# Kernel optimization log

Measured on AMD Instinct MI355X. Metric: run time of the kernel, lower is better.

Reference implementation:

```python
import jax, jax.numpy as jnp
import numpy as np

B, T = 4, 15
NY = NX = 256
RES = 0.05
LAT0 = 32.0
G = 9.81
F0 = 1e-4
C0 = 2.7
DT = 21600.0
TINT = 86400.0
NSTEP = int(TINT // DT)  # 4 Euler sub-steps

# --- grid spacing: mean of dx, dy as in lonlat2dxdy (uniform lon/lat grid) ---
_lat = LAT0 + RES * np.arange(NX, dtype=np.float64)  # lat varies along axis 1
_dx_mean = RES * 111000.0
_dy_mean = RES * 111000.0 * np.mean(np.cos(np.deg2rad(_lat)))
DX = np.float32(0.5 * (_dx_mean + _dy_mean))

# --- Helmholtz operator in DST-I space, shape (NY-2, NX-2) (square grid) ---
_i = np.arange(1, NX - 1, dtype=np.float64)
_j = np.arange(1, NY - 1, dtype=np.float64)
_X, _Y = np.meshgrid(_i, _j, indexing='ij')
_lap = (2 * (np.cos(np.pi / (NX - 1) * _X) - 1) / DX**2
        + 2 * (np.cos(np.pi / (NY - 1) * _Y) - 1) / DX**2)
HELM = jnp.asarray((G / F0) * _lap - G * F0 / C0**2, dtype=jnp.float32)

# --- boundary masks (SSH=None -> no NaN land mask; ind0 is empty) ---
_m = np.full((NY, NX), 3, dtype=np.int32)
_m[0, :] = _m[:, 0] = _m[-1, :] = _m[:, -1] = 1
_m[1, 1:-1] = 2; _m[1:-1, 1] = 2
_m[-2, 1:-1] = 2; _m[-3, 1:-1] = 2
_m[1:-1, -2] = 2; _m[1:-1, -3] = 2
IND12 = jnp.asarray((_m == 1) | (_m == 2))


def dstI1D(x):
    """1D type-I discrete sine transform along last axis."""
    n = x.shape[-1]
    xp = jnp.pad(x, [(0, 0)] * (x.ndim - 1) + [(1, 1)])
    return jnp.fft.irfft(-1j * xp, norm='ortho')[..., 1:n + 1]


def dstI2D(x):
    return jnp.swapaxes(dstI1D(jnp.swapaxes(dstI1D(x), -1, -2)), -1, -2)


def h2uv(h):
    """SSH -> geostrophic (u, v). f is the constant F0."""
    u = jnp.zeros_like(h).at[..., 1:-1, 1:].set(
        -G / F0 * (h[..., 2:, :-1] + h[..., 2:, 1:] - h[..., :-2, 1:] - h[..., :-2, :-1]) / (4 * DX))
    v = jnp.zeros_like(h).at[..., 1:, 1:-1].set(
        G / F0 * (h[..., 1:, 2:] + h[..., :-1, 2:] - h[..., :-1, :-2] - h[..., 1:, :-2]) / (4 * DX))
    return u, v


def h2pv(h, hbc):
    """SSH -> potential vorticity with boundary values from hbc on ind1|ind2."""
    interior = (G / F0 * ((h[..., 2:, 1:-1] + h[..., :-2, 1:-1] - 2 * h[..., 1:-1, 1:-1]) / DX**2
                          + (h[..., 1:-1, 2:] + h[..., 1:-1, :-2] - 2 * h[..., 1:-1, 1:-1]) / DX**2)
                - G * F0 / C0**2 * h[..., 1:-1, 1:-1])
    q = jnp.zeros_like(h).at[..., 1:-1, 1:-1].set(interior)
    return jnp.where(IND12, -G * F0 / C0**2 * hbc, q)


def _adv(up, vp, um, vm, v0):
    """3rd-order upwind advection."""
    c = 1.0 / (6 * DX)
    inner = (
        -up[..., 1:-1, 1:-1] * c * (2 * v0[..., 2:-2, 3:-1] + 3 * v0[..., 2:-2, 2:-2] - 6 * v0[..., 2:-2, 1:-3] + v0[..., 2:-2, :-4])
        + um[..., 1:-1, 1:-1] * c * (v0[..., 2:-2, 4:] - 6 * v0[..., 2:-2, 3:-1] + 3 * v0[..., 2:-2, 2:-2] + 2 * v0[..., 2:-2, 1:-3])
        - vp[..., 1:-1, 1:-1] * c * (2 * v0[..., 3:-1, 2:-2] + 3 * v0[..., 2:-2, 2:-2] - 6 * v0[..., 1:-3, 2:-2] + v0[..., :-4, 2:-2])
        + vm[..., 1:-1, 1:-1] * c * (v0[..., 4:, 2:-2] - 6 * v0[..., 3:-1, 2:-2] + 3 * v0[..., 2:-2, 2:-2] + 2 * v0[..., 1:-3, 2:-2]))
    return jnp.zeros_like(v0).at[..., 2:-2, 2:-2].set(inner)


def rhs(u, v, q0, way=1.0):
    uT = way * 0.5 * (u[..., 1:-1, 1:-1] + u[..., 1:-1, 2:])
    vT = way * 0.5 * (v[..., 1:-1, 1:-1] + v[..., 2:, 1:-1])
    up = jnp.maximum(uT, 0.0); um = jnp.minimum(uT, 0.0)
    vp = jnp.maximum(vT, 0.0); vm = jnp.minimum(vT, 0.0)
    r = _adv(up, vp, um, vm, q0)
    # beta term is identically zero: f = F0 is spatially constant. Kdiffus=None.
    return jnp.where(IND12, 0.0, r)


def pv2h(q, hb, qb):
    """PV -> SSH via DST-based inverse Helmholtz solve."""
    qin = q[..., 1:-1, 1:-1] - qb[..., 1:-1, 1:-1]
    inv = dstI2D(dstI2D(qin) / HELM)
    return jnp.zeros_like(q).at[..., 1:-1, 1:-1].set(inv) + hb


def conv2d(x, w, b):
    y = jax.lax.conv_general_dilated(x, w, (1, 1), 'SAME',
                                     dimension_numbers=('NCHW', 'OIHW', 'NCHW'))
    return y + b[None, :, None, None]


def qg_forecast(x):
    """One-day QG forecast of each frame from the previous one (NSTEP Euler sub-steps)."""
    h0 = x[:, :-1]            # [B, T-1, NY, NX]
    hb = h0                    # background / boundary SSH
    qb = h2pv(hb, hb)

    def body(carry, _):
        h, q = carry
        u, v = h2uv(h)
        q1 = q + DT * rhs(u, v, q)
        h1 = pv2h(q1, hb, qb)
        return (h1, q1), None

    (hf, _), _ = jax.lax.scan(body, (h0, qb), None, length=NSTEP)
    return hf


def setup_inputs() -> dict:
    key = jax.random.key(0)
    ks = jax.random.split(key, 8)
    s = 0.05
    return {
        'x': jax.random.normal(ks[0], (B, T, NY, NX), jnp.float32),
        'w_in': s * jax.random.normal(ks[1], (64, T, 3, 3), jnp.float32),
        'b_in': jnp.zeros((64,), jnp.float32),
        'w_hid': s * jax.random.normal(ks[2], (64, 64, 3, 3), jnp.float32),
        'b_hid': jnp.zeros((64,), jnp.float32),
        'w_b1': s * jax.random.normal(ks[3], (64, 64, 3, 3), jnp.float32),
        'b_b1': jnp.zeros((64,), jnp.float32),
        'w_b21': s * jax.random.normal(ks[4], (64, 64, 3, 3), jnp.float32),
        'b_b21': jnp.zeros((64,), jnp.float32),
        'w_b22': s * jax.random.normal(ks[5], (64, 64, 3, 3), jnp.float32),
        'b_b22': jnp.zeros((64,), jnp.float32),
        'w_out': s * jax.random.normal(ks[6], (T, 128, 3, 3), jnp.float32),
        'b_out': jnp.zeros((T,), jnp.float32),
    }


def reference(x, w_in, b_in, w_hid, b_hid, w_b1, b_b1, w_b21, b_b21,
              w_b22, b_b22, w_out, b_out):
    # QG dynamical prior cost
    hf = qg_forecast(x)
    dyn_cost = jnp.mean((x[:, 1:] - hf) ** 2)
    # bilinear AE prior cost (bilin_quad=False -> product of two branches)
    z = conv2d(x, w_in, b_in)
    z = conv2d(jax.nn.relu(z), w_hid, b_hid)
    nonlin = conv2d(z, w_b21, b_b21) * conv2d(z, w_b22, b_b22)
    xa = conv2d(jnp.concatenate([conv2d(z, w_b1, b_b1), nonlin], axis=1), w_out, b_out)
    ae_cost = jnp.mean((x - xa) ** 2)
    return dyn_cost + ae_cost
```

## Files before the change

kernel.cpp:

```cpp
#include <hip/hip_runtime.h>
#include <math.h>

#define NS 56
#define NPIX 65536

static constexpr double D_PI = 3.14159265358979323846;

typedef __attribute__((ext_vector_type(8))) short short8;
typedef __attribute__((ext_vector_type(4))) float f32x4;
typedef __attribute__((ext_vector_type(16))) float f32x16;

__device__ inline unsigned short f2bf(float f) {
  union { float f; unsigned int u; } v; v.f = f;
  unsigned int r = v.u + 0x7FFFu + ((v.u >> 16) & 1u);
  return (unsigned short)(r >> 16);
}
__device__ inline float bf2f(unsigned short b) {
  union { float f; unsigned int u; } v; v.u = ((unsigned int)b) << 16;
  return v.f;
}

#define SLC      (NS * NPIX)
#define OFF_PART 0
#define OFF_CNT  3584
#define OFF_S    4096
#define OFF_HM   36864
#define OFF_H    102400
#define OFF_QB   (OFF_H + SLC)
#define OFF_DQ0  (OFF_QB + SLC)
#define OFF_DQ1  (OFF_DQ0 + SLC / 2)
#define OFF_A1   (OFF_DQ1 + SLC / 2)
#define OFF_XP   (OFF_A1 + SLC / 2)
#define OFF_Z1   (OFF_XP + 2097152)
#define OFF_Z2   (OFF_Z1 + 8388608)
#define OFF_BC   (OFF_Z2 + 8388608)
#define OFF_XA   (OFF_BC + 8388608)
#define OFF_WT   (OFF_XA + 2097152)
#define W_IN    0
#define W_HID   10240
#define W_B1    47104
#define W_B21   83968
#define W_B22   120832
#define W_O1    157696
#define W_O2    166912

#define QCLAMP 1.0e12f
#define HCLAMP 1.0e15f

__global__ __launch_bounds__(256) void k_preamble(const float* __restrict__ x,
                                                  const float* __restrict__ w_in,
                                                  const float* __restrict__ w_hid,
                                                  const float* __restrict__ w_b1,
                                                  const float* __restrict__ w_b21,
                                                  const float* __restrict__ w_b22,
                                                  const float* __restrict__ w_out,
                                                  unsigned short* __restrict__ S,
                                                  float* __restrict__ HM,
                                                  unsigned short* __restrict__ wtb,
                                                  float* __restrict__ h,
                                                  float* __restrict__ qb,
                                                  unsigned short* __restrict__ xp,
                                                  unsigned int* __restrict__ cnt,
                                                  float dx2, float gf, float gfc) {
  const int blk = blockIdx.x;
  const int tid = threadIdx.x;
  if (blk < 256) {
    int idx = blk * 256 + tid;
    if (idx == 0) *cnt = 0u;
    int i = idx >> 8, j = idx & 255;
    float sv = 0.f, hv = 1.f;
    if (i < 254 && j < 254) {
      double arg = D_PI * (double)((i + 1) * (j + 1)) / 255.0;
      sv = (float)((2.0 / sqrt(510.0)) * sin(arg));
      double la = 2.0 * (cos(D_PI * (double)(i + 1) / 255.0) - 1.0) / (double)dx2
                + 2.0 * (cos(D_PI * (double)(j + 1) / 255.0) - 1.0) / (double)dx2;
      hv = (float)((9.81 / 1e-4) * la - 9.81 * 1e-4 / (2.7 * 2.7));
    }
    S[idx] = f2bf(sv);
    HM[idx] = hv;
  } else if (blk < 256 + 1008) {
    int jb = blk - 256;
    int job = jb / 144;
    int e = (jb - job * 144) * 256 + tid;
    const float* src;
    int dstOff, chunks, icpShift, icw, ic0, icReal, ocw, ocReal;
    switch (job) {
      case 0: src = w_in;  dstOff = W_IN;  chunks = 5;  icpShift = 4; icw = 15;  ic0 = 0;  icReal = 15; ocw = 64; ocReal = 64; break;
      case 1: src = w_hid; dstOff = W_HID; chunks = 18; icpShift = 6; icw = 64;  ic0 = 0;  icReal = 64; ocw = 64; ocReal = 64; break;
      case 2: src = w_b1;  dstOff = W_B1;  chunks = 18; icpShift = 6; icw = 64;  ic0 = 0;  icReal = 64; ocw = 64; ocReal = 64; break;
      case 3: src = w_b21; dstOff = W_B21; chunks = 18; icpShift = 6; icw = 64;  ic0 = 0;  icReal = 64; ocw = 64; ocReal = 64; break;
      case 4: src = w_b22; dstOff = W_B22; chunks = 18; icpShift = 6; icw = 64;  ic0 = 0;  icReal = 64; ocw = 64; ocReal = 64; break;
      case 5: src = w_out; dstOff = W_O1;  chunks = 18; icpShift = 6; icw = 128; ic0 = 0;  icReal = 64; ocw = 16; ocReal = 15; break;
      default: src = w_out; dstOff = W_O2; chunks = 18; icpShift = 6; icw = 128; ic0 = 64; icReal = 64; ocw = 16; ocReal = 15; break;
    }
    int total = chunks * 4 * ocw * 8;
    if (e < total) {
      int j = e & 7;
      int oc = (e >> 3) % ocw;
      int ckg = e / (8 * ocw);
      int kg = ckg & 3, c = ckg >> 2;
      int Kidx = c * 32 + kg * 8 + j;
      int tap = Kidx >> icpShift;
      int ic = Kidx & ((1 << icpShift) - 1);
      float v = 0.f;
      if (tap < 9 && ic < icReal && oc < ocReal)
        v = src[((size_t)oc * icw + ic0 + ic) * 9 + tap];
      wtb[dstOff + e] = f2bf(v);
    }
  } else if (blk < 256 + 1008 + 14336) {
    int idx = (blk - 1264) * 256 + tid;
    int s = idx >> 16, p = idx & 65535;
    int y = p >> 8, xx = p & 255;
    int b = s / 14, t = s - b * 14;
    const float* hb = x + (size_t)(b * 15 + t) * NPIX;
    float hc = hb[p];
    float qv;
    if (y >= 2 && y <= 252 && xx >= 2 && xx <= 252) {
      qv = gf * ((hb[p + 256] + hb[p - 256] - 2.f * hc) / dx2
               + (hb[p + 1] + hb[p - 1] - 2.f * hc) / dx2) - gfc * hc;
    } else {
      qv = -gfc * hc;
    }
    h[idx] = hc;
    qb[idx] = qv;
  } else {
    int e = (blk - 15600) * 256 + tid;
    int b = e >> 16, p = e & 65535;
    const float* xb = x + (size_t)b * 15 * NPIX + p;
    union { unsigned short u16[16]; uint4 u4[2]; } vv;
#pragma unroll
    for (int c = 0; c < 15; ++c) vv.u16[c] = f2bf(xb[(size_t)c * NPIX]);
    vv.u16[15] = 0;
    uint4* dst = (uint4*)&xp[(size_t)e * 16];
    dst[0] = vv.u4[0];
    dst[1] = vv.u4[1];
  }
}

template <bool FIRST>
__global__ __launch_bounds__(256) void k_qrhs_dq(const float* __restrict__ h,
                                                 const float* __restrict__ qbb,
                                                 const unsigned short* __restrict__ dqin,
                                                 unsigned short* __restrict__ dqout,
                                                 float ngf, float pgf, float fdx,
                                                 float cc, float dtf) {
  int idx = blockIdx.x * 256 + threadIdx.x;
  int s = idx >> 16, p = idx & 65535;
  int y = p >> 8, xx = p & 255;
  const float* H = h + (size_t)s * NPIX;
  const float* QB = qbb + (size_t)s * NPIX;
  const unsigned short* DQ = FIRST ? nullptr : dqin + (size_t)s * NPIX;
  auto dq = [&](int yy, int xc) -> float {
    if (FIRST) return 0.f;
    if (yy < 1 || yy > 254 || xc < 1 || xc > 254) return 0.f;
    return bf2f(DQ[(yy - 1) * 256 + (xc - 1)]);
  };
  float q1mqb = 0.f;
  if (y >= 2 && y <= 252 && xx >= 2 && xx <= 252) {
    float hSW = H[p + 255], hS = H[p + 256], hSE = H[p + 257];
    float hNW = H[p - 257], hN = H[p - 256], hNE = H[p - 255];
    float hW = H[p - 1], hE = H[p + 1];
    float uA = ngf * (hSW + hS - hN - hNW) / fdx;
    float uB = ngf * (hS + hSE - hNE - hN) / fdx;
    float vA = pgf * (hE + hNE - hNW - hW) / fdx;
    float vB = pgf * (hSE + hE - hW - hSW) / fdx;
    float uT = 0.5f * (uA + uB);
    float vT = 0.5f * (vA + vB);
    float up = fmaxf(uT, 0.f), um = fminf(uT, 0.f);
    float vp = fmaxf(vT, 0.f), vm = fminf(vT, 0.f);
    float qbc = QB[p];
    float Q0 = qbc + dq(y, xx);
    float QE = QB[p + 1] + dq(y, xx + 1), QW = QB[p - 1] + dq(y, xx - 1);
    float QEE = QB[p + 2] + dq(y, xx + 2), QWW = QB[p - 2] + dq(y, xx - 2);
    float QS = QB[p + 256] + dq(y + 1, xx), QN = QB[p - 256] + dq(y - 1, xx);
    float QSS = QB[p + 512] + dq(y + 2, xx), QNN = QB[p - 512] + dq(y - 2, xx);
    float r = -up * cc * (2.f * QE + 3.f * Q0 - 6.f * QW + QWW)
            + um * cc * (QEE - 6.f * QE + 3.f * Q0 + 2.f * QW)
            - vp * cc * (2.f * QS + 3.f * Q0 - 6.f * QN + QNN)
            + vm * cc * (QSS - 6.f * QS + 3.f * Q0 + 2.f * QN);
    float q1 = Q0 + dtf * r;
    q1 = fminf(fmaxf(q1, -QCLAMP), QCLAMP);
    q1mqb = q1 - qbc;
  }
  int wy = (y == 0) ? 254 : ((y == 255) ? 255 : y - 1);
  int wx = (xx == 0) ? 254 : ((xx == 255) ? 255 : xx - 1);
  dqout[(size_t)s * NPIX + wy * 256 + wx] = f2bf(q1mqb);
}

template <int EPI>
__global__ __launch_bounds__(512) void k_solve(const unsigned short* __restrict__ Sm,
                                               const unsigned short* __restrict__ Xb,
                                               unsigned short* __restrict__ Ob,
                                               const float* __restrict__ HM,
                                               const float* __restrict__ xin,
                                               float* __restrict__ hout) {
  __shared__ unsigned short Ul[32 * 256];
  const int s = blockIdx.x, q = blockIdx.y;
  const unsigned short* X = Xb + (size_t)s * NPIX;
  const int lane = threadIdx.x & 63, w = threadIdx.x >> 6;
  const int r31 = lane & 31, kh = lane >> 5;

  f32x16 acc;
#pragma unroll
  for (int i = 0; i < 16; ++i) acc[i] = 0.f;
  {
    const int ar = (32 * q + r31) * 256;
    const int br = (32 * w + r31) * 256;
#pragma unroll 4
    for (int kc = 0; kc < 256; kc += 16) {
      short8 a = *(const short8*)&Sm[ar + kc + kh * 8];
      short8 b = *(const short8*)&X[br + kc + kh * 8];
      acc = __builtin_amdgcn_mfma_f32_32x32x16_bf16(a, b, acc, 0, 0, 0);
    }
  }
  {
    const int col = 32 * w + r31;
    const int g = col >> 3, c7 = col & 7;
#pragma unroll
    for (int reg = 0; reg < 16; ++reg) {
      int i = (reg & 3) + 8 * (reg >> 2) + 4 * kh;
      Ul[i * 256 + (((g ^ (i & 7)) << 3) | c7)] = f2bf(acc[reg]);
    }
  }
  __syncthreads();

  f32x16 acc2;
#pragma unroll
  for (int i = 0; i < 16; ++i) acc2[i] = 0.f;
  {
    const int ar = (32 * w + r31) * 256;
    const int urow = r31 * 256;
    const int x7 = (r31 & 7);
#pragma unroll 4
    for (int kc = 0; kc < 256; kc += 16) {
      int g0 = (kc >> 3) + kh;
      short8 a = *(const short8*)&Sm[ar + kc + kh * 8];
      short8 b = *(const short8*)&Ul[urow + ((g0 ^ x7) << 3)];
      acc2 = __builtin_amdgcn_mfma_f32_32x32x16_bf16(a, b, acc2, 0, 0, 0);
    }
  }
  const int gn = 32 * q + r31;
  if (EPI == 0) {
    unsigned short* O = Ob + (size_t)s * NPIX;
#pragma unroll
    for (int reg = 0; reg < 16; ++reg) {
      int gm = 32 * w + (reg & 3) + 8 * (reg >> 2) + 4 * kh;
      O[(size_t)gm * 256 + gn] = f2bf(acc2[reg] / HM[(size_t)gm * 256 + gn]);
    }
  } else {
    int b = s / 14, t = s - b * 14;
    const float* hb = xin + (size_t)(b * 15 + t) * NPIX;
    float* H = hout + (size_t)s * NPIX;
    if (gn < 254) {
#pragma unroll
      for (int reg = 0; reg < 16; ++reg) {
        int gm = 32 * w + (reg & 3) + 8 * (reg >> 2) + 4 * kh;
        if (gm < 254) {
          size_t o = (size_t)(gm + 1) * 256 + (gn + 1);
          float hv = acc2[reg] + hb[o];
          H[o] = fminf(fmaxf(hv, -HCLAMP), HCLAMP);
        }
      }
    }
  }
}

template <int NSRC, int NOC, int OCF, bool RELU, int EMODE, int WSTRIDE>
__global__ __launch_bounds__(256) void k_conv64(const unsigned short* __restrict__ in0,
                                                const unsigned short* __restrict__ in1,
                                                const unsigned short* __restrict__ wt,
                                                const float* __restrict__ bias, int ocReal,
                                                const unsigned short* __restrict__ other,
                                                unsigned short* __restrict__ out) {
  constexpr int OCW = NOC * 16;
  __shared__ unsigned short tile[324 * 64];

  const int tid = threadIdx.x;
  const int lane = tid & 63, wave = tid >> 6;
  const int cl = lane & 15, kg = lane >> 4;
  const int b = blockIdx.z;
  const int gx0 = blockIdx.x * 16, gy0 = blockIdx.y * 16;

  f32x4 acc[4][NOC];
#pragma unroll
  for (int j = 0; j < NOC; ++j) {
    int oc = j * 16 + cl;
    float bv = (bias != nullptr && oc < ocReal) ? bias[oc] : 0.f;
#pragma unroll
    for (int i = 0; i < 4; ++i) acc[i][j] = (f32x4){bv, bv, bv, bv};
  }

  for (int src = 0; src < NSRC; ++src) {
    const unsigned short* inb = (src ? in1 : in0) + (size_t)b * NPIX * 64;
    const unsigned short* wtp = wt + src * WSTRIDE;
    if (src) __syncthreads();
    for (int c = tid; c < 2592; c += 256) {
      int pp = c >> 3, g = c & 7;
      int ly = pp / 18, lx = pp - ly * 18;
      int iy = gy0 + ly - 1, ix = gx0 + lx - 1;
      uint4 v = make_uint4(0u, 0u, 0u, 0u);
      if (iy >= 0 && iy < 256 && ix >= 0 && ix < 256)
        v = *(const uint4*)&inb[((size_t)iy * 256 + ix) * 64 + g * 8];
      int sw = g ^ (pp & 7);
      *(uint4*)&tile[pp * 64 + sw * 8] = v;
    }
    __syncthreads();
#pragma unroll 3
    for (int cm = 0; cm < 18; ++cm) {
      const int tap = cm >> 1;
      const int g = (cm & 1) * 4 + kg;
      const int dy = tap / 3, dxx = tap - dy * 3;
      short8 bfr[NOC];
#pragma unroll
      for (int j = 0; j < NOC; ++j)
        bfr[j] = *(const short8*)&wtp[(((size_t)cm * 4 + kg) * OCW + j * 16 + cl) * 8];
      const int tc = cl + dxx;
#pragma unroll
      for (int i = 0; i < 4; ++i) {
        int pp = (wave * 4 + i + dy) * 18 + tc;
        int g2 = g ^ (pp & 7);
        short8 av = *(const short8*)&tile[pp * 64 + g2 * 8];
#pragma unroll
        for (int j = 0; j < NOC; ++j)
          acc[i][j] = __builtin_amdgcn_mfma_f32_16x16x32_bf16(av, bfr[j], acc[i][j], 0, 0, 0);
      }
    }
  }

  const size_t outBase = (size_t)b * NPIX * OCF;
#pragma unroll
  for (int i = 0; i < 4; ++i) {
    int y = gy0 + wave * 4 + i;
#pragma unroll
    for (int j = 0; j < NOC; ++j) {
      int oc = j * 16 + cl;
#pragma unroll
      for (int r = 0; r < 4; ++r) {
        int px = gx0 + kg * 4 + r;
        size_t oi = outBase + ((size_t)y * 256 + px) * OCF + oc;
        float v = acc[i][j][r];
        if (EMODE == 1) v *= bf2f(other[oi]);
        if (RELU) v = fmaxf(v, 0.f);
        out[oi] = f2bf(v);
      }
    }
  }
}

__global__ __launch_bounds__(256) void k_convmul(const unsigned short* __restrict__ in,
                                                 const unsigned short* __restrict__ wtA,
                                                 const unsigned short* __restrict__ wtB,
                                                 const float* __restrict__ biasA,
                                                 const float* __restrict__ biasB,
                                                 unsigned short* __restrict__ out) {
  __shared__ unsigned short tile[324 * 64];
  const int tid = threadIdx.x;
  const int lane = tid & 63, wave = tid >> 6;
  const int cl = lane & 15, kg = lane >> 4;
  const int b = blockIdx.z;
  const int gx0 = blockIdx.x * 16, gy0 = blockIdx.y * 16;

  f32x4 accA[4][4], accB[4][4];
#pragma unroll
  for (int j = 0; j < 4; ++j) {
    float ba = biasA[j * 16 + cl], bb = biasB[j * 16 + cl];
#pragma unroll
    for (int i = 0; i < 4; ++i) {
      accA[i][j] = (f32x4){ba, ba, ba, ba};
      accB[i][j] = (f32x4){bb, bb, bb, bb};
    }
  }

  const unsigned short* inb = in + (size_t)b * NPIX * 64;
  for (int c = tid; c < 2592; c += 256) {
    int pp = c >> 3, g = c & 7;
    int ly = pp / 18, lx = pp - ly * 18;
    int iy = gy0 + ly - 1, ix = gx0 + lx - 1;
    uint4 v = make_uint4(0u, 0u, 0u, 0u);
    if (iy >= 0 && iy < 256 && ix >= 0 && ix < 256)
      v = *(const uint4*)&inb[((size_t)iy * 256 + ix) * 64 + g * 8];
    int sw = g ^ (pp & 7);
    *(uint4*)&tile[pp * 64 + sw * 8] = v;
  }
  __syncthreads();

#pragma unroll 2
  for (int cm = 0; cm < 18; ++cm) {
    const int tap = cm >> 1;
    const int g = (cm & 1) * 4 + kg;
    const int dy = tap / 3, dxx = tap - dy * 3;
    const int tc = cl + dxx;
    short8 av[4];
#pragma unroll
    for (int i = 0; i < 4; ++i) {
      int pp = (wave * 4 + i + dy) * 18 + tc;
      int g2 = g ^ (pp & 7);
      av[i] = *(const short8*)&tile[pp * 64 + g2 * 8];
    }
#pragma unroll
    for (int j = 0; j < 4; ++j) {
      short8 wa = *(const short8*)&wtA[(((size_t)cm * 4 + kg) * 64 + j * 16 + cl) * 8];
#pragma unroll
      for (int i = 0; i < 4; ++i)
        accA[i][j] = __builtin_amdgcn_mfma_f32_16x16x32_bf16(av[i], wa, accA[i][j], 0, 0, 0);
    }
#pragma unroll
    for (int j = 0; j < 4; ++j) {
      short8 wb = *(const short8*)&wtB[(((size_t)cm * 4 + kg) * 64 + j * 16 + cl) * 8];
#pragma unroll
      for (int i = 0; i < 4; ++i)
        accB[i][j] = __builtin_amdgcn_mfma_f32_16x16x32_bf16(av[i], wb, accB[i][j], 0, 0, 0);
    }
  }

  const size_t outBase = (size_t)b * NPIX * 64;
#pragma unroll
  for (int i = 0; i < 4; ++i) {
    int y = gy0 + wave * 4 + i;
#pragma unroll
    for (int j = 0; j < 4; ++j) {
      int oc = j * 16 + cl;
#pragma unroll
      for (int r = 0; r < 4; ++r) {
        int px = gx0 + kg * 4 + r;
        size_t oi = outBase + ((size_t)y * 256 + px) * 64 + oc;
        out[oi] = f2bf(accA[i][j][r] * accB[i][j][r]);
      }
    }
  }
}

__global__ __launch_bounds__(256) void k_conv16(const unsigned short* __restrict__ in,
                                                const unsigned short* __restrict__ wt,
                                                const float* __restrict__ bias,
                                                unsigned short* __restrict__ out) {
  __shared__ unsigned short wlds[10240];
  __shared__ unsigned short tile[324 * 16];

  const int tid = threadIdx.x;
  const int lane = tid & 63, wave = tid >> 6;
  const int cl = lane & 15, kg = lane >> 4;
  const int b = blockIdx.z;
  const int gx0 = blockIdx.x * 16, gy0 = blockIdx.y * 16;

  {
    uint4* wl = (uint4*)wlds;
    const uint4* wg = (const uint4*)wt;
    for (int i = tid; i < 1280; i += 256) wl[i] = wg[i];
  }
  const unsigned short* inb = in + (size_t)b * NPIX * 16;
  for (int c = tid; c < 648; c += 256) {
    int pp = c >> 1, g = c & 1;
    int ly = pp / 18, lx = pp - ly * 18;
    int iy = gy0 + ly - 1, ix = gx0 + lx - 1;
    uint4 v = make_uint4(0u, 0u, 0u, 0u);
    if (iy >= 0 && iy < 256 && ix >= 0 && ix < 256)
      v = *(const uint4*)&inb[((size_t)iy * 256 + ix) * 16 + g * 8];
    int sw = g ^ (pp & 1);
    *(uint4*)&tile[pp * 16 + sw * 8] = v;
  }
  __syncthreads();

  f32x4 acc[4][4];
#pragma unroll
  for (int j = 0; j < 4; ++j) {
    float bv = bias[j * 16 + cl];
#pragma unroll
    for (int i = 0; i < 4; ++i) acc[i][j] = (f32x4){bv, bv, bv, bv};
  }

#pragma unroll
  for (int c = 0; c < 5; ++c) {
    int tap = 2 * c + (kg >> 1);
    int dy = tap / 3, dxx = tap - dy * 3;
    int gidx = kg & 1;
    short8 bfr[4];
#pragma unroll
    for (int j = 0; j < 4; ++j)
      bfr[j] = *(const short8*)&wlds[((c * 4 + kg) * 64 + j * 16 + cl) * 8];
    int tc = cl + dxx;
#pragma unroll
    for (int i = 0; i < 4; ++i) {
      int tr = wave * 4 + i + dy;
      if (tr > 17) tr = 17;
      int pp = tr * 18 + tc;
      int g2 = gidx ^ (pp & 1);
      short8 av = *(const short8*)&tile[pp * 16 + g2 * 8];
#pragma unroll
      for (int j = 0; j < 4; ++j)
        acc[i][j] = __builtin_amdgcn_mfma_f32_16x16x32_bf16(av, bfr[j], acc[i][j], 0, 0, 0);
    }
  }

  const size_t outBase = (size_t)b * NPIX * 64;
#pragma unroll
  for (int i = 0; i < 4; ++i) {
    int y = gy0 + wave * 4 + i;
#pragma unroll
    for (int j = 0; j < 4; ++j) {
      int oc = j * 16 + cl;
#pragma unroll
      for (int r = 0; r < 4; ++r) {
        int px = gx0 + kg * 4 + r;
        size_t oi = outBase + ((size_t)y * 256 + px) * 64 + oc;
        out[oi] = f2bf(fmaxf(acc[i][j][r], 0.f));
      }
    }
  }
}

__global__ __launch_bounds__(256) void k_red_all(const float* __restrict__ x,
                                                 const float* __restrict__ h,
                                                 const unsigned short* __restrict__ xa,
                                                 double* __restrict__ part,
                                                 unsigned int* __restrict__ cnt,
                                                 float* __restrict__ out) {
  const int NB1 = 1024, NBT = 1536;
  const int bid = blockIdx.x;
  const int tid = threadIdx.x;
  double sum = 0.0;
  if (bid < NB1) {
    for (int e = bid * 256 + tid; e < NS * NPIX; e += NB1 * 256) {
      int s = e >> 16, p = e & 65535;
      int b = s / 14, t = s - b * 14;
      float d = x[(size_t)(b * 15 + t + 1) * NPIX + p] - h[e];
      sum += (double)d * (double)d;
    }
  } else {
    for (int e = (bid - NB1) * 256 + tid; e < 60 * NPIX; e += (NBT - NB1) * 256) {
      int b = e / (15 * NPIX);
      int r2 = e - b * 15 * NPIX;
      int c = r2 >> 16, p = r2 & 65535;
      float xav = bf2f(xa[((size_t)b * NPIX + p) * 16 + c]);
      float d = x[e] - xav;
      sum += (double)d * (double)d;
    }
  }
  for (int o = 32; o > 0; o >>= 1) sum += __shfl_down(sum, o);
  __shared__ double sw[4];
  __shared__ bool last;
  int lane = tid & 63, wid = tid >> 6;
  if (lane == 0) sw[wid] = sum;
  __syncthreads();
  if (tid == 0) {
    part[bid] = sw[0] + sw[1] + sw[2] + sw[3];
    __threadfence();
    unsigned int t = atomicAdd(cnt, 1u);
    last = (t == (unsigned)(NBT - 1));
  }
  __syncthreads();
  if (last) {
    __threadfence();
    double s1 = 0.0, s2 = 0.0;
    for (int i = tid; i < NBT; i += 256) {
      if (i < NB1) s1 += part[i]; else s2 += part[i];
    }
    for (int o = 32; o > 0; o >>= 1) {
      s1 += __shfl_down(s1, o);
      s2 += __shfl_down(s2, o);
    }
    __shared__ double a1[4], a2[4];
    if (lane == 0) { a1[wid] = s1; a2[wid] = s2; }
    __syncthreads();
    if (tid == 0) {
      double v = (a1[0] + a1[1] + a1[2] + a1[3]) / (double)(NS * NPIX)
               + (a2[0] + a2[1] + a2[2] + a2[3]) / (double)(60 * NPIX);
      if (!(v == v)) v = 0.0;
      if (v > 1.0e30) v = 1.0e30;
      if (v < -1.0e30) v = -1.0e30;
      out[0] = (float)v;
    }
  }
}

extern "C" void kernel_launch(void* const* d_in, const int* in_sizes, int n_in,
                              void* d_out, int out_size, void* d_ws, size_t ws_size,
                              hipStream_t stream) {
  (void)in_sizes; (void)n_in; (void)out_size; (void)ws_size;
  const float* x     = (const float*)d_in[0];
  const float* w_in  = (const float*)d_in[1];
  const float* b_in  = (const float*)d_in[2];
  const float* w_hid = (const float*)d_in[3];
  const float* b_hid = (const float*)d_in[4];
  const float* w_b1  = (const float*)d_in[5];
  const float* b_b1  = (const float*)d_in[6];
  const float* w_b21 = (const float*)d_in[7];
  const float* b_b21 = (const float*)d_in[8];
  const float* w_b22 = (const float*)d_in[9];
  const float* b_b22 = (const float*)d_in[10];
  const float* w_out = (const float*)d_in[11];
  const float* b_out = (const float*)d_in[12];
  float* ws = (float*)d_ws;
  float* out = (float*)d_out;

  double mc = 0.0;
  for (int k = 0; k < 256; ++k) mc += cos((32.0 + 0.05 * k) * D_PI / 180.0);
  mc /= 256.0;
  float DXf = (float)(0.5 * (5550.0 + 5550.0 * mc));
  float dx2 = DXf * DXf;
  float gf  = (float)(9.81 / 1e-4);
  float ngf = (float)(-9.81 / 1e-4);
  float gfc = (float)(9.81 * 1e-4 / (2.7 * 2.7));
  float fdx = 4.0f * DXf;
  float cc  = 1.0f / (6.0f * DXf);
  float dtf = 21600.0f;

  double* part = (double*)d_ws;
  unsigned int* cnt = (unsigned int*)(ws + OFF_CNT);
  unsigned short* S  = (unsigned short*)(ws + OFF_S);
  float* HM = ws + OFF_HM;
  float* h  = ws + OFF_H;
  float* qb = ws + OFF_QB;
  unsigned short* dq0 = (unsigned short*)(ws + OFF_DQ0);
  unsigned short* dq1 = (unsigned short*)(ws + OFF_DQ1);
  unsigned short* A1 = (unsigned short*)(ws + OFF_A1);
  unsigned short* xp = (unsigned short*)(ws + OFF_XP);
  unsigned short* z1 = (unsigned short*)(ws + OFF_Z1);
  unsigned short* z2 = (unsigned short*)(ws + OFF_Z2);
  unsigned short* bc = (unsigned short*)(ws + OFF_BC);
  unsigned short* xa = (unsigned short*)(ws + OFF_XA);
  unsigned short* wtb = (unsigned short*)(ws + OFF_WT);

  k_preamble<<<dim3(16624), dim3(256), 0, stream>>>(x, w_in, w_hid, w_b1, w_b21, w_b22,
                                                    w_out, S, HM, wtb, h, qb, xp, cnt,
                                                    dx2, gf, gfc);

  dim3 sg(56, 8);
  dim3 qg(NS * NPIX / 256);
  unsigned short* dqc = dq0;
  unsigned short* dqn = dq1;
  for (int step = 0; step < 4; ++step) {
    if (step == 0)
      k_qrhs_dq<true><<<qg, dim3(256), 0, stream>>>(h, qb, nullptr, dqc, ngf, gf, fdx, cc, dtf);
    else {
      k_qrhs_dq<false><<<qg, dim3(256), 0, stream>>>(h, qb, dqc, dqn, ngf, gf, fdx, cc, dtf);
      unsigned short* tmp = dqc; dqc = dqn; dqn = tmp;
    }
    k_solve<0><<<sg, dim3(512), 0, stream>>>(S, dqc, A1, HM, nullptr, nullptr);
    k_solve<1><<<sg, dim3(512), 0, stream>>>(S, A1, nullptr, nullptr, x, h);
  }

  dim3 cg4(16, 16, 4);
  k_conv16<<<cg4, dim3(256), 0, stream>>>(xp, wtb + W_IN, b_in, z1);
  k_conv64<1, 4, 64, false, 0, 0><<<cg4, dim3(256), 0, stream>>>(
      z1, z1, wtb + W_HID, b_hid, 64, nullptr, z2);
  k_conv64<1, 4, 64, false, 0, 0><<<cg4, dim3(256), 0, stream>>>(
      z2, z2, wtb + W_B1, b_b1, 64, nullptr, z1);
  k_convmul<<<cg4, dim3(256), 0, stream>>>(z2, wtb + W_B21, wtb + W_B22, b_b21, b_b22, bc);
  k_conv64<2, 1, 16, false, 0, 9216><<<cg4, dim3(256), 0, stream>>>(
      z1, bc, wtb + W_O1, b_out, 15, nullptr, xa);

  k_red_all<<<dim3(1536), dim3(256), 0, stream>>>(x, h, xa, part, cnt, out);
}
```

Baseline: 555.5 us.

## Double waves per block in conv kernels and simplify dq stencil indexing

New measurement: 505.0 us. -9.1%, faster.

```diff
diff --git a/kernel.cpp b/kernel.cpp
--- a/kernel.cpp
+++ b/kernel.cpp
@@ -149,11 +149,11 @@
   int y = p >> 8, xx = p & 255;
   const float* H = h + (size_t)s * NPIX;
   const float* QB = qbb + (size_t)s * NPIX;
-  const unsigned short* DQ = FIRST ? nullptr : dqin + (size_t)s * NPIX;
-  auto dq = [&](int yy, int xc) -> float {
+  const unsigned short* DQ = dqin + (size_t)s * NPIX;
+  const int base = p - 257;
+  auto dqv = [&](int d) -> float {
     if (FIRST) return 0.f;
-    if (yy < 1 || yy > 254 || xc < 1 || xc > 254) return 0.f;
-    return bf2f(DQ[(yy - 1) * 256 + (xc - 1)]);
+    return bf2f(DQ[(base + d) & 65535]);
   };
   float q1mqb = 0.f;
   if (y >= 2 && y <= 252 && xx >= 2 && xx <= 252) {
@@ -169,11 +169,11 @@
     float up = fmaxf(uT, 0.f), um = fminf(uT, 0.f);
     float vp = fmaxf(vT, 0.f), vm = fminf(vT, 0.f);
     float qbc = QB[p];
-    float Q0 = qbc + dq(y, xx);
-    float QE = QB[p + 1] + dq(y, xx + 1), QW = QB[p - 1] + dq(y, xx - 1);
-    float QEE = QB[p + 2] + dq(y, xx + 2), QWW = QB[p - 2] + dq(y, xx - 2);
-    float QS = QB[p + 256] + dq(y + 1, xx), QN = QB[p - 256] + dq(y - 1, xx);
-    float QSS = QB[p + 512] + dq(y + 2, xx), QNN = QB[p - 512] + dq(y - 2, xx);
+    float Q0 = qbc + dqv(0);
+    float QE = QB[p + 1] + dqv(1), QW = QB[p - 1] + dqv(-1);
+    float QEE = QB[p + 2] + dqv(2), QWW = QB[p - 2] + dqv(-2);
+    float QS = QB[p + 256] + dqv(256), QN = QB[p - 256] + dqv(-256);
+    float QSS = QB[p + 512] + dqv(512), QNN = QB[p - 512] + dqv(-512);
     float r = -up * cc * (2.f * QE + 3.f * Q0 - 6.f * QW + QWW)
             + um * cc * (QEE - 6.f * QE + 3.f * Q0 + 2.f * QW)
             - vp * cc * (2.f * QS + 3.f * Q0 - 6.f * QN + QNN)
@@ -265,79 +265,73 @@
   }
 }
 
-template <int NSRC, int NOC, int OCF, bool RELU, int EMODE, int WSTRIDE>
-__global__ __launch_bounds__(256) void k_conv64(const unsigned short* __restrict__ in0,
-                                                const unsigned short* __restrict__ in1,
-                                                const unsigned short* __restrict__ wt,
-                                                const float* __restrict__ bias, int ocReal,
-                                                const unsigned short* __restrict__ other,
-                                                unsigned short* __restrict__ out) {
-  constexpr int OCW = NOC * 16;
+template <bool RELU, int EMODE>
+__global__ __launch_bounds__(512) void k_conv64b(const unsigned short* __restrict__ in,
+                                                 const unsigned short* __restrict__ wt,
+                                                 const float* __restrict__ bias,
+                                                 const unsigned short* __restrict__ other,
+                                                 unsigned short* __restrict__ out) {
   __shared__ unsigned short tile[324 * 64];
-
   const int tid = threadIdx.x;
   const int lane = tid & 63, wave = tid >> 6;
   const int cl = lane & 15, kg = lane >> 4;
+  const int wrow = wave & 3, wh = wave >> 2;
   const int b = blockIdx.z;
   const int gx0 = blockIdx.x * 16, gy0 = blockIdx.y * 16;
 
-  f32x4 acc[4][NOC];
-#pragma unroll
-  for (int j = 0; j < NOC; ++j) {
-    int oc = j * 16 + cl;
-    float bv = (bias != nullptr && oc < ocReal) ? bias[oc] : 0.f;
+  f32x4 acc[4][2];
+#pragma unroll
+  for (int j = 0; j < 2; ++j) {
+    float bv = bias[wh * 32 + j * 16 + cl];
 #pragma unroll
     for (int i = 0; i < 4; ++i) acc[i][j] = (f32x4){bv, bv, bv, bv};
   }
 
-  for (int src = 0; src < NSRC; ++src) {
-    const unsigned short* inb = (src ? in1 : in0) + (size_t)b * NPIX * 64;
-    const unsigned short* wtp = wt + src * WSTRIDE;
-    if (src) __syncthreads();
-    for (int c = tid; c < 2592; c += 256) {
-      int pp = c >> 3, g = c & 7;
-      int ly = pp / 18, lx = pp - ly * 18;
-      int iy = gy0 + ly - 1, ix = gx0 + lx - 1;
-      uint4 v = make_uint4(0u, 0u, 0u, 0u);
-      if (iy >= 0 && iy < 256 && ix >= 0 && ix < 256)
-        v = *(const uint4*)&inb[((size_t)iy * 256 + ix) * 64 + g * 8];
-      int sw = g ^ (pp & 7);
-      *(uint4*)&tile[pp * 64 + sw * 8] = v;
-    }
-    __syncthreads();
+  const unsigned short* inb = in + (size_t)b * NPIX * 64;
+  for (int c = tid; c < 2592; c += 512) {
+    int pp = c >> 3, g = c & 7;
+    int ly = pp / 18, lx = pp - ly * 18;
+    int iy = gy0 + ly - 1, ix = gx0 + lx - 1;
+    uint4 v = make_uint4(0u, 0u, 0u, 0u);
+    if (iy >= 0 && iy < 256 && ix >= 0 && ix < 256)
+      v = *(const uint4*)&inb[((size_t)iy * 256 + ix) * 64 + g * 8];
+    int sw = g ^ (pp & 7);
+    *(uint4*)&tile[pp * 64 + sw * 8] = v;
+  }
+  __syncthreads();
+
 #pragma unroll 3
-    for (int cm = 0; cm < 18; ++cm) {
-      const int tap = cm >> 1;
-      const int g = (cm & 1) * 4 + kg;
-      const int dy = tap / 3, dxx = tap - dy * 3;
-      short8 bfr[NOC];
-#pragma unroll
-      for (int j = 0; j < NOC; ++j)
-        bfr[j] = *(const short8*)&wtp[(((size_t)cm * 4 + kg) * OCW + j * 16 + cl) * 8];
-      const int tc = cl + dxx;
-#pragma unroll
-      for (int i = 0; i < 4; ++i) {
-        int pp = (wave * 4 + i + dy) * 18 + tc;
-        int g2 = g ^ (pp & 7);
-        short8 av = *(const short8*)&tile[pp * 64 + g2 * 8];
-#pragma unroll
-        for (int j = 0; j < NOC; ++j)
-          acc[i][j] = __builtin_amdgcn_mfma_f32_16x16x32_bf16(av, bfr[j], acc[i][j], 0, 0, 0);
-      }
-    }
-  }
-
-  const size_t outBase = (size_t)b * NPIX * OCF;
+  for (int cm = 0; cm < 18; ++cm) {
+    const int tap = cm >> 1;
+    const int g = (cm & 1) * 4 + kg;
+    const int dy = tap / 3, dxx = tap - dy * 3;
+    short8 bfr[2];
+#pragma unroll
+    for (int j = 0; j < 2; ++j)
+      bfr[j] = *(const short8*)&wt[(((size_t)cm * 4 + kg) * 64 + wh * 32 + j * 16 + cl) * 8];
+    const int tc = cl + dxx;
+#pragma unroll
+    for (int i = 0; i < 4; ++i) {
+      int pp = (wrow * 4 + i + dy) * 18 + tc;
+      int g2 = g ^ (pp & 7);
+      short8 av = *(const short8*)&tile[pp * 64 + g2 * 8];
+#pragma unroll
+      for (int j = 0; j < 2; ++j)
+        acc[i][j] = __builtin_amdgcn_mfma_f32_16x16x32_bf16(av, bfr[j], acc[i][j], 0, 0, 0);
+    }
+  }
+
+  const size_t outBase = (size_t)b * NPIX * 64;
 #pragma unroll
   for (int i = 0; i < 4; ++i) {
-    int y = gy0 + wave * 4 + i;
-#pragma unroll
-    for (int j = 0; j < NOC; ++j) {
-      int oc = j * 16 + cl;
+    int y = gy0 + wrow * 4 + i;
+#pragma unroll
+    for (int j = 0; j < 2; ++j) {
+      int oc = wh * 32 + j * 16 + cl;
 #pragma unroll
       for (int r = 0; r < 4; ++r) {
         int px = gx0 + kg * 4 + r;
-        size_t oi = outBase + ((size_t)y * 256 + px) * OCF + oc;
+        size_t oi = outBase + ((size_t)y * 256 + px) * 64 + oc;
         float v = acc[i][j][r];
         if (EMODE == 1) v *= bf2f(other[oi]);
         if (RELU) v = fmaxf(v, 0.f);
@@ -347,7 +341,7 @@
   }
 }
 
-__global__ __launch_bounds__(256) void k_convmul(const unsigned short* __restrict__ in,
+__global__ __launch_bounds__(512) void k_convmul(const unsigned short* __restrict__ in,
                                                  const unsigned short* __restrict__ wtA,
                                                  const unsigned short* __restrict__ wtB,
                                                  const float* __restrict__ biasA,
@@ -357,13 +351,14 @@
   const int tid = threadIdx.x;
   const int lane = tid & 63, wave = tid >> 6;
   const int cl = lane & 15, kg = lane >> 4;
+  const int wrow = wave & 3, wh = wave >> 2;
   const int b = blockIdx.z;
   const int gx0 = blockIdx.x * 16, gy0 = blockIdx.y * 16;
 
-  f32x4 accA[4][4], accB[4][4];
-#pragma unroll
-  for (int j = 0; j < 4; ++j) {
-    float ba = biasA[j * 16 + cl], bb = biasB[j * 16 + cl];
+  f32x4 accA[4][2], accB[4][2];
+#pragma unroll
+  for (int j = 0; j < 2; ++j) {
+    float ba = biasA[wh * 32 + j * 16 + cl], bb = biasB[wh * 32 + j * 16 + cl];
 #pragma unroll
     for (int i = 0; i < 4; ++i) {
       accA[i][j] = (f32x4){ba, ba, ba, ba};
@@ -372,7 +367,7 @@
   }
 
   const unsigned short* inb = in + (size_t)b * NPIX * 64;
-  for (int c = tid; c < 2592; c += 256) {
+  for (int c = tid; c < 2592; c += 512) {
     int pp = c >> 3, g = c & 7;
     int ly = pp / 18, lx = pp - ly * 18;
     int iy = gy0 + ly - 1, ix = gx0 + lx - 1;
@@ -390,42 +385,102 @@
     const int g = (cm & 1) * 4 + kg;
     const int dy = tap / 3, dxx = tap - dy * 3;
     const int tc = cl + dxx;
-    short8 av[4];
+    short8 wa[2], wb[2];
+#pragma unroll
+    for (int j = 0; j < 2; ++j) {
+      wa[j] = *(const short8*)&wtA[(((size_t)cm * 4 + kg) * 64 + wh * 32 + j * 16 + cl) * 8];
+      wb[j] = *(const short8*)&wtB[(((size_t)cm * 4 + kg) * 64 + wh * 32 + j * 16 + cl) * 8];
+    }
 #pragma unroll
     for (int i = 0; i < 4; ++i) {
-      int pp = (wave * 4 + i + dy) * 18 + tc;
+      int pp = (wrow * 4 + i + dy) * 18 + tc;
       int g2 = g ^ (pp & 7);
-      av[i] = *(const short8*)&tile[pp * 64 + g2 * 8];
-    }
-#pragma unroll
-    for (int j = 0; j < 4; ++j) {
-      short8 wa = *(const short8*)&wtA[(((size_t)cm * 4 + kg) * 64 + j * 16 + cl) * 8];
-#pragma unroll
-      for (int i = 0; i < 4; ++i)
-        accA[i][j] = __builtin_amdgcn_mfma_f32_16x16x32_bf16(av[i], wa, accA[i][j], 0, 0, 0);
-    }
-#pragma unroll
-    for (int j = 0; j < 4; ++j) {
-      short8 wb = *(const short8*)&wtB[(((size_t)cm * 4 + kg) * 64 + j * 16 + cl) * 8];
-#pragma unroll
-      for (int i = 0; i < 4; ++i)
-        accB[i][j] = __builtin_amdgcn_mfma_f32_16x16x32_bf16(av[i], wb, accB[i][j], 0, 0, 0);
+      short8 av = *(const short8*)&tile[pp * 64 + g2 * 8];
+#pragma unroll
+      for (int j = 0; j < 2; ++j) {
+        accA[i][j] = __builtin_amdgcn_mfma_f32_16x16x32_bf16(av, wa[j], accA[i][j], 0, 0, 0);
+        accB[i][j] = __builtin_amdgcn_mfma_f32_16x16x32_bf16(av, wb[j], accB[i][j], 0, 0, 0);
+      }
     }
   }
 
   const size_t outBase = (size_t)b * NPIX * 64;
 #pragma unroll
   for (int i = 0; i < 4; ++i) {
-    int y = gy0 + wave * 4 + i;
-#pragma unroll
-    for (int j = 0; j < 4; ++j) {
-      int oc = j * 16 + cl;
+    int y = gy0 + wrow * 4 + i;
+#pragma unroll
+    for (int j = 0; j < 2; ++j) {
+      int oc = wh * 32 + j * 16 + cl;
 #pragma unroll
       for (int r = 0; r < 4; ++r) {
         int px = gx0 + kg * 4 + r;
         size_t oi = outBase + ((size_t)y * 256 + px) * 64 + oc;
         out[oi] = f2bf(accA[i][j][r] * accB[i][j][r]);
       }
+    }
+  }
+}
+
+__global__ __launch_bounds__(512) void k_convout(const unsigned short* __restrict__ in0,
+                                                 const unsigned short* __restrict__ in1,
+                                                 const unsigned short* __restrict__ wt,
+                                                 const float* __restrict__ bias,
+                                                 unsigned short* __restrict__ out) {
+  __shared__ unsigned short tile[324 * 64];
+  const int tid = threadIdx.x;
+  const int lane = tid & 63, wave = tid >> 6;
+  const int cl = lane & 15, kg = lane >> 4;
+  const int b = blockIdx.z;
+  const int gx0 = blockIdx.x * 16, gy0 = blockIdx.y * 16;
+
+  f32x4 acc[2];
+  {
+    float bv = (cl < 15) ? bias[cl] : 0.f;
+    acc[0] = (f32x4){bv, bv, bv, bv};
+    acc[1] = acc[0];
+  }
+
+  for (int src = 0; src < 2; ++src) {
+    const unsigned short* inb = (src ? in1 : in0) + (size_t)b * NPIX * 64;
+    const unsigned short* wtp = wt + src * 9216;
+    if (src) __syncthreads();
+    for (int c = tid; c < 2592; c += 512) {
+      int pp = c >> 3, g = c & 7;
+      int ly = pp / 18, lx = pp - ly * 18;
+      int iy = gy0 + ly - 1, ix = gx0 + lx - 1;
+      uint4 v = make_uint4(0u, 0u, 0u, 0u);
+      if (iy >= 0 && iy < 256 && ix >= 0 && ix < 256)
+        v = *(const uint4*)&inb[((size_t)iy * 256 + ix) * 64 + g * 8];
+      int sw = g ^ (pp & 7);
+      *(uint4*)&tile[pp * 64 + sw * 8] = v;
+    }
+    __syncthreads();
+#pragma unroll 3
+    for (int cm = 0; cm < 18; ++cm) {
+      const int tap = cm >> 1;
+      const int g = (cm & 1) * 4 + kg;
+      const int dy = tap / 3, dxx = tap - dy * 3;
+      short8 bfr = *(const short8*)&wtp[(((size_t)cm * 4 + kg) * 16 + cl) * 8];
+      const int tc = cl + dxx;
+#pragma unroll
+      for (int i = 0; i < 2; ++i) {
+        int pp = (wave * 2 + i + dy) * 18 + tc;
+        int g2 = g ^ (pp & 7);
+        short8 av = *(const short8*)&tile[pp * 64 + g2 * 8];
+        acc[i] = __builtin_amdgcn_mfma_f32_16x16x32_bf16(av, bfr, acc[i], 0, 0, 0);
+      }
+    }
+  }
+
+  const size_t outBase = (size_t)b * NPIX * 16;
+#pragma unroll
+  for (int i = 0; i < 2; ++i) {
+    int y = gy0 + wave * 2 + i;
+#pragma unroll
+    for (int r = 0; r < 4; ++r) {
+      int px = gx0 + kg * 4 + r;
+      size_t oi = outBase + ((size_t)y * 256 + px) * 16 + cl;
+      out[oi] = f2bf(acc[i][r]);
     }
   }
 }
@@ -631,7 +686,7 @@
   unsigned short* dqn = dq1;
   for (int step = 0; step < 4; ++step) {
     if (step == 0)
-      k_qrhs_dq<true><<<qg, dim3(256), 0, stream>>>(h, qb, nullptr, dqc, ngf, gf, fdx, cc, dtf);
+      k_qrhs_dq<true><<<qg, dim3(256), 0, stream>>>(h, qb, dq1, dqc, ngf, gf, fdx, cc, dtf);
     else {
       k_qrhs_dq<false><<<qg, dim3(256), 0, stream>>>(h, qb, dqc, dqn, ngf, gf, fdx, cc, dtf);
       unsigned short* tmp = dqc; dqc = dqn; dqn = tmp;
@@ -642,13 +697,10 @@
 
   dim3 cg4(16, 16, 4);
   k_conv16<<<cg4, dim3(256), 0, stream>>>(xp, wtb + W_IN, b_in, z1);
-  k_conv64<1, 4, 64, false, 0, 0><<<cg4, dim3(256), 0, stream>>>(
-      z1, z1, wtb + W_HID, b_hid, 64, nullptr, z2);
-  k_conv64<1, 4, 64, false, 0, 0><<<cg4, dim3(256), 0, stream>>>(
-      z2, z2, wtb + W_B1, b_b1, 64, nullptr, z1);
-  k_convmul<<<cg4, dim3(256), 0, stream>>>(z2, wtb + W_B21, wtb + W_B22, b_b21, b_b22, bc);
-  k_conv64<2, 1, 16, false, 0, 9216><<<cg4, dim3(256), 0, stream>>>(
-      z1, bc, wtb + W_O1, b_out, 15, nullptr, xa);
+  k_conv64b<false, 0><<<cg4, dim3(512), 0, stream>>>(z1, wtb + W_HID, b_hid, nullptr, z2);
+  k_conv64b<false, 0><<<cg4, dim3(512), 0, stream>>>(z2, wtb + W_B1, b_b1, nullptr, z1);
+  k_convmul<<<cg4, dim3(512), 0, stream>>>(z2, wtb + W_B21, wtb + W_B22, b_b21, b_b22, bc);
+  k_convout<<<cg4, dim3(512), 0, stream>>>(z1, bc, wtb + W_O1, b_out, xa);
 
   k_red_all<<<dim3(1536), dim3(256), 0, stream>>>(x, h, xa, part, cnt, out);
 }
```
